# Optimization experiments

Measured on AMD Instinct MI355X. Metric: run time of the kernel, lower is better.

Reference implementation:

```python
import jax, jax.numpy as jnp
import numpy as np

TOP_K = 2  # module uses global top_k=2

def setup_inputs() -> dict:
    key = jax.random.key(0)
    k1, k2, k3 = jax.random.split(key, 3)
    B, S, D, E = 4, 4096, 2048, 64
    x = jax.random.normal(k1, (B, S, D), dtype=jnp.float32)
    W = jax.random.normal(k2, (E, D), dtype=jnp.float32) * 0.02  # gate_linear weight (no bias)
    noise_weight = jnp.zeros((E,), dtype=jnp.float32)  # nn.Parameter(torch.zeros(E))
    noise = jax.random.normal(k3, (B, S, E), dtype=jnp.float32)  # randn_like(logits) * noisy_std(=1.0)
    return {"x": x, "W": W, "noise_weight": noise_weight, "noise": noise}

def reference(x, W, noise_weight, noise):
    # logits = gate_linear(x)
    logits = jnp.einsum('bsd,ed->bse', x, W)
    # noisy logits: noise * noise_weight (per-expert scale), added to logits
    logits_noisy = logits + noise * noise_weight
    # top-k (largest, sorted descending, like torch.topk)
    top_vals, top_idx = jax.lax.top_k(logits_noisy, TOP_K)  # [B,S,k]
    B, S, E = logits_noisy.shape
    # scatter top-k values into -inf tensor along expert dim
    sparse = jnp.full_like(logits_noisy, -jnp.inf)
    b_ix = jnp.arange(B)[:, None, None]
    s_ix = jnp.arange(S)[None, :, None]
    sparse = sparse.at[b_ix, s_ix, top_idx].set(top_vals)
    # softmax over experts; exp(-inf)=0 zeros out non-selected experts
    gated_probs = jax.nn.softmax(sparse, axis=-1)
    return (gated_probs, top_idx, top_vals)
```

## Files before the change

### kernel.cpp

```cpp
#include <hip/hip_runtime.h>
#include <math.h>


typedef __attribute__((ext_vector_type(8))) __bf16 bf16x8;
typedef __attribute__((ext_vector_type(8))) unsigned short u16x8;
typedef __attribute__((ext_vector_type(4))) float f32x4;

constexpr int EXPN = 64;
constexpr int TM   = 16;
constexpr int BK   = 32;

__device__ __forceinline__ void split2(float f, unsigned short& h, unsigned short& l) {
    const unsigned b = __float_as_uint(f);
    h = (unsigned short)(b >> 16);
    const float fh = __uint_as_float(b & 0xffff0000u);
    l = (unsigned short)(__float_as_uint(f - fh) >> 16);
}

__device__ __forceinline__ bf16x8 as_bf16(u16x8 v) {
    union { u16x8 u; bf16x8 b; } c; c.u = v; return c.b;
}

__device__ __forceinline__ void gload16(const void* g, void* l) {
    typedef __attribute__((address_space(1))) void gv;
    typedef __attribute__((address_space(3))) void lv;
    __builtin_amdgcn_global_load_lds((gv*)g, (lv*)l, 16, 0, 0);
}

__global__ __launch_bounds__(256)
void convert_w_kernel(const float* __restrict__ W,
                      unsigned short* __restrict__ whp,
                      unsigned short* __restrict__ wlp, int n4)
{
    const int i = blockIdx.x * 256 + threadIdx.x;
    if (i >= n4) return;
    const float4 v = *(const float4*)(W + (size_t)i * 4);
    const float f[4] = {v.x, v.y, v.z, v.w};
    unsigned short h[4], l[4];
#pragma unroll
    for (int j = 0; j < 4; ++j) split2(f[j], h[j], l[j]);
    *(ushort4*)(whp + (size_t)i * 4) = make_ushort4(h[0], h[1], h[2], h[3]);
    *(ushort4*)(wlp + (size_t)i * 4) = make_ushort4(l[0], l[1], l[2], l[3]);
}

__global__ __launch_bounds__(256, 6)
void moe_gate_kernel(const float* __restrict__ x,
                     const float* __restrict__ W,
                     const unsigned short* __restrict__ whp,
                     const unsigned short* __restrict__ wlp,
                     const float* __restrict__ nw,
                     const float* __restrict__ noise,
                     float* __restrict__ probs,
                     float* __restrict__ idx_out,
                     float* __restrict__ val_out,
                     int D)
{
    __shared__ float          xs[2][TM][BK];
    __shared__ unsigned short ws[2][EXPN][2 * BK];
    __shared__ float          ls[TM][EXPN + 1];

    const int tid  = threadIdx.x;
    const int lane = tid & 63;
    const int wv   = tid >> 6;
    const int m0   = blockIdx.x * TM;

    const int fr = lane & 15;
    const int kq = (lane >> 4) * 8;
    const int er = wv * 16 + fr;

    const int sl8 = lane >> 3;
    const int gl  = lane & 7;
    const int j0 = wv * 2, j1 = j0 + 1;
    const int e0 = j0 * 8 + sl8, e1 = j1 * 8 + sl8;
    const int g0 = gl ^ (e0 & 7), g1 = gl ^ (e1 & 7);
    const unsigned short* wsrc0 = (g0 < 4)
        ? whp + (size_t)e0 * D + g0 * 8
        : wlp + (size_t)e0 * D + (g0 - 4) * 8;
    const unsigned short* wsrc1 = (g1 < 4)
        ? whp + (size_t)e1 * D + g1 * 8
        : wlp + (size_t)e1 * D + (g1 - 4) * 8;
    const float* xsrc = nullptr;
    if (wv >= 2) {
        const int row = (wv - 2) * 8 + sl8;
        const int gx  = gl ^ (row & 7);
        xsrc = x + (size_t)(m0 + row) * D + gx * 4;
    }

#define STAGE(b, c) {                                                        \
        gload16(wsrc0 + (size_t)(c) * BK, &ws[b][0][0] + j0 * 512);          \
        gload16(wsrc1 + (size_t)(c) * BK, &ws[b][0][0] + j1 * 512);          \
        if (wv >= 2)                                                         \
            gload16(xsrc + (size_t)(c) * BK, &xs[b][0][0] + (wv - 2) * 256); \
    }

    f32x4 acc = {0.f, 0.f, 0.f, 0.f};

#define COMPUTE(b) {                                                              \
        const char* xbp = (const char*)&xs[b][0][0];                              \
        const char* wbp = (const char*)&ws[b][0][0];                              \
        const float4 xa  = *(const float4*)(xbp + fr * 128 + (((kq >> 2)    ) ^ (fr & 7)) * 16); \
        const float4 xc  = *(const float4*)(xbp + fr * 128 + (((kq >> 2) + 1) ^ (fr & 7)) * 16); \
        const u16x8  bhv = *(const u16x8*)(wbp + er * 128 + (((kq >> 3)    ) ^ (fr & 7)) * 16); \
        const u16x8  blv = *(const u16x8*)(wbp + er * 128 + (((kq >> 3) + 4) ^ (fr & 7)) * 16); \
        const float xf[8] = {xa.x, xa.y, xa.z, xa.w, xc.x, xc.y, xc.z, xc.w};     \
        u16x8 hv, lv;                                                             \
        _Pragma("unroll")                                                         \
        for (int i_ = 0; i_ < 8; ++i_) {                                          \
            unsigned short h_, l_; split2(xf[i_], h_, l_);                        \
            hv[i_] = h_; lv[i_] = l_;                                             \
        }                                                                         \
        const bf16x8 ah = as_bf16(hv), al = as_bf16(lv);                          \
        acc = __builtin_amdgcn_mfma_f32_16x16x32_bf16(ah, as_bf16(bhv), acc, 0, 0, 0); \
        acc = __builtin_amdgcn_mfma_f32_16x16x32_bf16(ah, as_bf16(blv), acc, 0, 0, 0); \
        acc = __builtin_amdgcn_mfma_f32_16x16x32_bf16(al, as_bf16(bhv), acc, 0, 0, 0); \
    }

    const int nchunk = D / BK;
    STAGE(0, 0)
    __syncthreads();

    for (int c = 0; c < nchunk; ++c) {
        if (c & 1) {
            if (c + 1 < nchunk) STAGE(0, c + 1)
            COMPUTE(1)
        } else {
            if (c + 1 < nchunk) STAGE(1, c + 1)
            COMPUTE(0)
        }
        __syncthreads();
    }

#undef STAGE
#undef COMPUTE

    const int trow = (lane >> 4) * 4;
#pragma unroll
    for (int r = 0; r < 4; ++r)
        ls[trow + r][wv * 16 + fr] = acc[r];
    __syncthreads();

    const float nwv = nw[lane];

#pragma unroll 1
    for (int t = 0; t < 4; ++t) {
        const int tl = wv * 4 + t;
        const int g  = m0 + tl;
        const float logit = fmaf(noise[(size_t)g * EXPN + lane], nwv, ls[tl][lane]);

        float v0; int i0;
        {
            float v = logit; int ix = lane;
#pragma unroll
            for (int off = 32; off; off >>= 1) {
                const float vo = __shfl_xor(v, off);
                const int   io = __shfl_xor(ix, off);
                if (vo > v || (vo == v && io < ix)) { v = vo; ix = io; }
            }
            v0 = v; i0 = ix;
        }
        float v1; int i1;
        {
            float v = (lane == i0) ? -INFINITY : logit; int ix = lane;
#pragma unroll
            for (int off = 32; off; off >>= 1) {
                const float vo = __shfl_xor(v, off);
                const int   io = __shfl_xor(ix, off);
                if (vo > v || (vo == v && io < ix)) { v = vo; ix = io; }
            }
            v1 = v; i1 = ix;
        }
        float v2; int i2;
        {
            float v = (lane == i0 || lane == i1) ? -INFINITY : logit; int ix = lane;
#pragma unroll
            for (int off = 32; off; off >>= 1) {
                const float vo = __shfl_xor(v, off);
                const int   io = __shfl_xor(ix, off);
                if (vo > v || (vo == v && io < ix)) { v = vo; ix = io; }
            }
            v2 = v; i2 = ix;
        }

        const float eps = 1e-3f;
        if ((v0 - v1) < eps || (v1 - v2) < eps) {
            const float* xr  = x + (size_t)g * D;
            const float* w0r = W + (size_t)i0 * D;
            const float* w1r = W + (size_t)i1 * D;
            const float* w2r = W + (size_t)i2 * D;
            double s0 = 0.0, s1 = 0.0, s2 = 0.0;
            for (int d = lane; d < D; d += 64) {
                const double xv = (double)xr[d];
                s0 += xv * (double)w0r[d];
                s1 += xv * (double)w1r[d];
                s2 += xv * (double)w2r[d];
            }
#pragma unroll
            for (int off = 32; off; off >>= 1) {
                s0 += __shfl_xor(s0, off);
                s1 += __shfl_xor(s1, off);
                s2 += __shfl_xor(s2, off);
            }
            double d0 = s0 + (double)noise[(size_t)g * EXPN + i0] * (double)nw[i0];
            double d1 = s1 + (double)noise[(size_t)g * EXPN + i1] * (double)nw[i1];
            double d2 = s2 + (double)noise[(size_t)g * EXPN + i2] * (double)nw[i2];
            #define CSWAP(va, ia, vb, ib)                                   \
                if ((vb > va) || (vb == va && ib < ia)) {                   \
                    double tv = va; va = vb; vb = tv;                       \
                    int ti = ia; ia = ib; ib = ti; }
            CSWAP(d0, i0, d1, i1)
            CSWAP(d1, i1, d2, i2)
            CSWAP(d0, i0, d1, i1)
            #undef CSWAP
            v0 = (float)d0; v1 = (float)d1;
        }

        const float e1  = expf(v1 - v0);
        const float inv = 1.0f / (1.0f + e1);

        float p = 0.f;
        if (lane == i0)      p = inv;
        else if (lane == i1) p = e1 * inv;
        probs[(size_t)g * EXPN + lane] = p;

        if (lane == 0) {
            idx_out[(size_t)g * 2 + 0] = (float)i0;
            idx_out[(size_t)g * 2 + 1] = (float)i1;
            val_out[(size_t)g * 2 + 0] = v0;
            val_out[(size_t)g * 2 + 1] = v1;
        }
    }
}

extern "C" void kernel_launch(void* const* d_in, const int* in_sizes, int n_in,
                              void* d_out, int out_size, void* d_ws, size_t ws_size,
                              hipStream_t stream) {
    const float* x     = (const float*)d_in[0];
    const float* W     = (const float*)d_in[1];
    const float* nw    = (const float*)d_in[2];
    const float* noise = (const float*)d_in[3];

    const int M = in_sizes[3] / EXPN;
    const int D = in_sizes[0] / M;
    const int wn = in_sizes[1];

    unsigned short* whp = (unsigned short*)d_ws;
    unsigned short* wlp = whp + (size_t)wn;

    float* probs   = (float*)d_out;
    float* idx_out = probs + (size_t)M * EXPN;
    float* val_out = idx_out + (size_t)M * 2;

    const int n4 = wn / 4;
    convert_w_kernel<<<(n4 + 255) / 256, 256, 0, stream>>>(W, whp, wlp, n4);

    const int grid = M / TM;
    moe_gate_kernel<<<grid, 256, 0, stream>>>(x, W, whp, wlp, nw, noise,
                                              probs, idx_out, val_out, D);
}
```

Baseline: 256.8 us.

## Enlarge tiles, use 512-thread blocks, triple-buffer loads with vmcnt waits

Raises the row tile from 16 to 32 tokens and the K chunk from 32 to 64, and launches 512 threads per block (two token halves times four expert quarters). The double buffer with a full __syncthreads every chunk becomes a three-stage ring that keeps two chunks of global-to-LDS loads in flight, using explicit s_waitcnt vmcnt plus a bare barrier. The aim is to hide load latency better and halve the number of barriers. In exchange there are fewer blocks, more LDS per block and lower occupancy. The epilogue must also cover 32 rows, and part of that code is not visible.

After: 222.7 us. 13.3% less time.

```diff
diff --git a/kernel.cpp b/kernel.cpp
--- a/kernel.cpp
+++ b/kernel.cpp
@@ -7,8 +7,11 @@
 typedef __attribute__((ext_vector_type(4))) float f32x4;
 
 constexpr int EXPN = 64;
-constexpr int TM   = 16;
-constexpr int BK   = 32;
+constexpr int TM   = 32;
+constexpr int BK   = 64;
+constexpr int WBYTES = EXPN * 2 * BK * 2;
+constexpr int XBYTES = TM * BK * 4;
+constexpr int BUFB   = WBYTES + XBYTES;
 
 __device__ __forceinline__ void split2(float f, unsigned short& h, unsigned short& l) {
     const unsigned b = __float_as_uint(f);
@@ -43,7 +46,7 @@
     *(ushort4*)(wlp + (size_t)i * 4) = make_ushort4(l[0], l[1], l[2], l[3]);
 }
 
-__global__ __launch_bounds__(256, 6)
+__global__ __launch_bounds__(512, 4)
 void moe_gate_kernel(const float* __restrict__ x,
                      const float* __restrict__ W,
                      const unsigned short* __restrict__ whp,
@@ -55,88 +58,90 @@
                      float* __restrict__ val_out,
                      int D)
 {
-    __shared__ float          xs[2][TM][BK];
-    __shared__ unsigned short ws[2][EXPN][2 * BK];
-    __shared__ float          ls[TM][EXPN + 1];
+    __shared__ __align__(16) char smem[3 * BUFB];
 
     const int tid  = threadIdx.x;
     const int lane = tid & 63;
     const int wv   = tid >> 6;
+    const int th   = wv >> 2;
+    const int eq   = wv & 3;
     const int m0   = blockIdx.x * TM;
 
     const int fr = lane & 15;
     const int kq = (lane >> 4) * 8;
-    const int er = wv * 16 + fr;
-
-    const int sl8 = lane >> 3;
-    const int gl  = lane & 7;
+    const int f7 = fr & 7;
+
+    const int sl   = lane >> 4;
+    const int slot = lane & 15;
     const int j0 = wv * 2, j1 = j0 + 1;
-    const int e0 = j0 * 8 + sl8, e1 = j1 * 8 + sl8;
-    const int g0 = gl ^ (e0 & 7), g1 = gl ^ (e1 & 7);
-    const unsigned short* wsrc0 = (g0 < 4)
-        ? whp + (size_t)e0 * D + g0 * 8
-        : wlp + (size_t)e0 * D + (g0 - 4) * 8;
-    const unsigned short* wsrc1 = (g1 < 4)
-        ? whp + (size_t)e1 * D + g1 * 8
-        : wlp + (size_t)e1 * D + (g1 - 4) * 8;
-    const float* xsrc = nullptr;
-    if (wv >= 2) {
-        const int row = (wv - 2) * 8 + sl8;
-        const int gx  = gl ^ (row & 7);
-        xsrc = x + (size_t)(m0 + row) * D + gx * 4;
-    }
-
-#define STAGE(b, c) {                                                        \
-        gload16(wsrc0 + (size_t)(c) * BK, &ws[b][0][0] + j0 * 512);          \
-        gload16(wsrc1 + (size_t)(c) * BK, &ws[b][0][0] + j1 * 512);          \
-        if (wv >= 2)                                                         \
-            gload16(xsrc + (size_t)(c) * BK, &xs[b][0][0] + (wv - 2) * 256); \
+    const int we0 = j0 * 4 + sl, we1 = j1 * 4 + sl;
+    const int wg0 = slot ^ (we0 & 7), wg1 = slot ^ (we1 & 7);
+    const unsigned short* wsrc0 = ((wg0 < 8) ? whp : wlp)
+                                + (size_t)we0 * D + (wg0 & 7) * 8;
+    const unsigned short* wsrc1 = ((wg1 < 8) ? whp : wlp)
+                                + (size_t)we1 * D + (wg1 & 7) * 8;
+    const int xrow = wv * 4 + sl;
+    const int xg   = slot ^ (xrow & 7);
+    const float* xsrc = x + (size_t)(m0 + xrow) * D + xg * 4;
+
+#define STAGE(b, c) {                                                     \
+        char* bb_ = smem + (b) * BUFB;                                    \
+        gload16(wsrc0 + (size_t)(c) * BK, bb_ + j0 * 1024);               \
+        gload16(wsrc1 + (size_t)(c) * BK, bb_ + j1 * 1024);               \
+        gload16(xsrc  + (size_t)(c) * BK, bb_ + WBYTES + wv * 1024);      \
     }
 
     f32x4 acc = {0.f, 0.f, 0.f, 0.f};
 
 #define COMPUTE(b) {                                                              \
-        const char* xbp = (const char*)&xs[b][0][0];                              \
-        const char* wbp = (const char*)&ws[b][0][0];                              \
-        const float4 xa  = *(const float4*)(xbp + fr * 128 + (((kq >> 2)    ) ^ (fr & 7)) * 16); \
-        const float4 xc  = *(const float4*)(xbp + fr * 128 + (((kq >> 2) + 1) ^ (fr & 7)) * 16); \
-        const u16x8  bhv = *(const u16x8*)(wbp + er * 128 + (((kq >> 3)    ) ^ (fr & 7)) * 16); \
-        const u16x8  blv = *(const u16x8*)(wbp + er * 128 + (((kq >> 3) + 4) ^ (fr & 7)) * 16); \
-        const float xf[8] = {xa.x, xa.y, xa.z, xa.w, xc.x, xc.y, xc.z, xc.w};     \
-        u16x8 hv, lv;                                                             \
+        const char* wbp_ = smem + (b) * BUFB;                                     \
+        const char* xbp_ = wbp_ + WBYTES;                                         \
         _Pragma("unroll")                                                         \
-        for (int i_ = 0; i_ < 8; ++i_) {                                          \
-            unsigned short h_, l_; split2(xf[i_], h_, l_);                        \
-            hv[i_] = h_; lv[i_] = l_;                                             \
+        for (int ks_ = 0; ks_ < 2; ++ks_) {                                       \
+            const int kk_ = ks_ * 32 + kq;                                        \
+            const int sx_ = (kk_ >> 2) ^ f7;            \
+            const float4 xa_ = *(const float4*)(xbp_ + (th*16+fr)*256 + sx_*16);  \
+            const float4 xc_ = *(const float4*)(xbp_ + (th*16+fr)*256 + (sx_^1)*16); \
+            const int gh_ = kk_ >> 3;                                             \
+            const u16x8 bh_ = *(const u16x8*)(wbp_ + (eq*16+fr)*256 + (gh_ ^ f7)*16); \
+            const u16x8 bl_ = *(const u16x8*)(wbp_ + (eq*16+fr)*256 + (8 + (gh_ ^ f7))*16); \
+            const float xf_[8] = {xa_.x, xa_.y, xa_.z, xa_.w,                     \
+                                  xc_.x, xc_.y, xc_.z, xc_.w};                    \
+            u16x8 hv_, lv_;                                                       \
+            _Pragma("unroll")                                                     \
+            for (int i_ = 0; i_ < 8; ++i_) {                                      \
+                unsigned short h_, l_; split2(xf_[i_], h_, l_);                   \
+                hv_[i_] = h_; lv_[i_] = l_;                                       \
+            }                                                                     \
+            const bf16x8 ah_ = as_bf16(hv_), al_ = as_bf16(lv_);                  \
+            acc = __builtin_amdgcn_mfma_f32_16x16x32_bf16(ah_, as_bf16(bh_), acc, 0, 0, 0); \
+            acc = __builtin_amdgcn_mfma_f32_16x16x32_bf16(ah_, as_bf16(bl_), acc, 0, 0, 0); \
+            acc = __builtin_amdgcn_mfma_f32_16x16x32_bf16(al_, as_bf16(bh_), acc, 0, 0, 0); \
         }                                                                         \
-        const bf16x8 ah = as_bf16(hv), al = as_bf16(lv);                          \
-        acc = __builtin_amdgcn_mfma_f32_16x16x32_bf16(ah, as_bf16(bhv), acc, 0, 0, 0); \
-        acc = __builtin_amdgcn_mfma_f32_16x16x32_bf16(ah, as_bf16(blv), acc, 0, 0, 0); \
-        acc = __builtin_amdgcn_mfma_f32_16x16x32_bf16(al, as_bf16(bhv), acc, 0, 0, 0); \
     }
 
     const int nchunk = D / BK;
     STAGE(0, 0)
-    __syncthreads();
+    STAGE(1, 1)
 
     for (int c = 0; c < nchunk; ++c) {
-        if (c & 1) {
-            if (c + 1 < nchunk) STAGE(0, c + 1)
-            COMPUTE(1)
-        } else {
-            if (c + 1 < nchunk) STAGE(1, c + 1)
-            COMPUTE(0)
-        }
-        __syncthreads();
+        if (c < nchunk - 1) asm volatile("s_waitcnt vmcnt(3)" ::: "memory");
+        else                asm volatile("s_waitcnt vmcnt(0)" ::: "memory");
+        __builtin_amdgcn_s_barrier();
+        if (c + 2 < nchunk) STAGE((c + 2) % 3, c + 2)
+        COMPUTE(c % 3)
     }
 
 #undef STAGE
 #undef COMPUTE
 
-    const int trow = (lane >> 4) * 4;
+    __syncthreads();
+
+    float (*ls)[EXPN + 1] = (float (*)[EXPN + 1])smem;
+    const int trow = th * 16 + (lane >> 4) * 4;
 #pragma unroll
     for (int r = 0; r < 4; ++r)
-        ls[trow + r][wv * 16 + fr] = acc[r];
+        ls[trow + r][eq * 16 + fr] = acc[r];
     __syncthreads();
 
     const float nwv = nw[lane];
@@ -254,6 +259,6 @@
     convert_w_kernel<<<(n4 + 255) / 256, 256, 0, stream>>>(W, whp, wlp, n4);
 
     const int grid = M / TM;
-    moe_gate_kernel<<<grid, 256, 0, stream>>>(x, W, whp, wlp, nw, noise,
+    moe_gate_kernel<<<grid, 512, 0, stream>>>(x, W, whp, wlp, nw, noise,
                                               probs, idx_out, val_out, D);
 }
```

## Enlarge gate GEMM tile to 64 tokens with split-K across 16 waves

Applied to the files above, without the earlier changes.

Moves from 16-token, 4-wave blocks to 64-token, 1024-thread blocks. Each wave computes a 2x2 set of 16x16 MFMA tiles over one quarter of a 128-wide K chunk, and the four K-partials are reduced through shared memory at the end. The larger tile reuses each staged W chunk across four times as many tokens, cutting redundant W traffic and barrier count per FLOP. The bf16 hi/lo split of x now uses byte-permute packing. The costs are much more LDS per block, lower occupancy, and a full vmcnt drain at every barrier.

After: 215.1 us. -16.2%, faster.

```diff
diff --git a/kernel.cpp b/kernel.cpp
--- a/kernel.cpp
+++ b/kernel.cpp
@@ -5,10 +5,15 @@
 typedef __attribute__((ext_vector_type(8))) __bf16 bf16x8;
 typedef __attribute__((ext_vector_type(8))) unsigned short u16x8;
 typedef __attribute__((ext_vector_type(4))) float f32x4;
+typedef __attribute__((ext_vector_type(4))) unsigned u32x4;
 
 constexpr int EXPN = 64;
-constexpr int TM   = 16;
-constexpr int BK   = 32;
+constexpr int TM   = 64;
+constexpr int BK   = 128;
+constexpr int WCH  = EXPN * BK * 2 * 2;
+constexpr int XCH  = TM * BK * 4;
+constexpr int BUF  = WCH + XCH;
+constexpr int NBUF = 2;
 
 __device__ __forceinline__ void split2(float f, unsigned short& h, unsigned short& l) {
     const unsigned b = __float_as_uint(f);
@@ -19,6 +24,34 @@
 
 __device__ __forceinline__ bf16x8 as_bf16(u16x8 v) {
     union { u16x8 u; bf16x8 b; } c; c.u = v; return c.b;
+}
+__device__ __forceinline__ bf16x8 as_bf16_u32(u32x4 v) {
+    union { u32x4 u; bf16x8 b; } c; c.u = v; return c.b;
+}
+
+__device__ __forceinline__ void split_pack(float4 a, float4 c, bf16x8& hi, bf16x8& lo) {
+    const unsigned u0=__float_as_uint(a.x), u1=__float_as_uint(a.y),
+                   u2=__float_as_uint(a.z), u3=__float_as_uint(a.w),
+                   u4=__float_as_uint(c.x), u5=__float_as_uint(c.y),
+                   u6=__float_as_uint(c.z), u7=__float_as_uint(c.w);
+    u32x4 hp, lp;
+    hp[0] = __builtin_amdgcn_perm(u1, u0, 0x07060302u);
+    hp[1] = __builtin_amdgcn_perm(u3, u2, 0x07060302u);
+    hp[2] = __builtin_amdgcn_perm(u5, u4, 0x07060302u);
+    hp[3] = __builtin_amdgcn_perm(u7, u6, 0x07060302u);
+    const unsigned d0=__float_as_uint(a.x-__uint_as_float(u0&0xffff0000u));
+    const unsigned d1=__float_as_uint(a.y-__uint_as_float(u1&0xffff0000u));
+    const unsigned d2=__float_as_uint(a.z-__uint_as_float(u2&0xffff0000u));
+    const unsigned d3=__float_as_uint(a.w-__uint_as_float(u3&0xffff0000u));
+    const unsigned d4=__float_as_uint(c.x-__uint_as_float(u4&0xffff0000u));
+    const unsigned d5=__float_as_uint(c.y-__uint_as_float(u5&0xffff0000u));
+    const unsigned d6=__float_as_uint(c.z-__uint_as_float(u6&0xffff0000u));
+    const unsigned d7=__float_as_uint(c.w-__uint_as_float(u7&0xffff0000u));
+    lp[0] = __builtin_amdgcn_perm(d1, d0, 0x07060302u);
+    lp[1] = __builtin_amdgcn_perm(d3, d2, 0x07060302u);
+    lp[2] = __builtin_amdgcn_perm(d5, d4, 0x07060302u);
+    lp[3] = __builtin_amdgcn_perm(d7, d6, 0x07060302u);
+    hi = as_bf16_u32(hp); lo = as_bf16_u32(lp);
 }
 
 __device__ __forceinline__ void gload16(const void* g, void* l) {
@@ -43,7 +76,9 @@
     *(ushort4*)(wlp + (size_t)i * 4) = make_ushort4(l[0], l[1], l[2], l[3]);
 }
 
-__global__ __launch_bounds__(256, 6)
+#define MFMA16(a, b, c) __builtin_amdgcn_mfma_f32_16x16x32_bf16((a), (b), (c), 0, 0, 0)
+
+__global__ __launch_bounds__(1024, 4)
 void moe_gate_kernel(const float* __restrict__ x,
                      const float* __restrict__ W,
                      const unsigned short* __restrict__ whp,
@@ -55,88 +90,111 @@
                      float* __restrict__ val_out,
                      int D)
 {
-    __shared__ float          xs[2][TM][BK];
-    __shared__ unsigned short ws[2][EXPN][2 * BK];
-    __shared__ float          ls[TM][EXPN + 1];
+    __shared__ __align__(16) char smem[NBUF * BUF];
 
     const int tid  = threadIdx.x;
     const int lane = tid & 63;
     const int wv   = tid >> 6;
+    const int kw   = wv >> 2;
+    const int th   = (wv >> 1) & 1;
+    const int eh   = wv & 1;
     const int m0   = blockIdx.x * TM;
 
-    const int fr = lane & 15;
-    const int kq = (lane >> 4) * 8;
-    const int er = wv * 16 + fr;
-
-    const int sl8 = lane >> 3;
-    const int gl  = lane & 7;
-    const int j0 = wv * 2, j1 = j0 + 1;
-    const int e0 = j0 * 8 + sl8, e1 = j1 * 8 + sl8;
-    const int g0 = gl ^ (e0 & 7), g1 = gl ^ (e1 & 7);
-    const unsigned short* wsrc0 = (g0 < 4)
-        ? whp + (size_t)e0 * D + g0 * 8
-        : wlp + (size_t)e0 * D + (g0 - 4) * 8;
-    const unsigned short* wsrc1 = (g1 < 4)
-        ? whp + (size_t)e1 * D + g1 * 8
-        : wlp + (size_t)e1 * D + (g1 - 4) * 8;
-    const float* xsrc = nullptr;
-    if (wv >= 2) {
-        const int row = (wv - 2) * 8 + sl8;
-        const int gx  = gl ^ (row & 7);
-        xsrc = x + (size_t)(m0 + row) * D + gx * 4;
-    }
-
-#define STAGE(b, c) {                                                        \
-        gload16(wsrc0 + (size_t)(c) * BK, &ws[b][0][0] + j0 * 512);          \
-        gload16(wsrc1 + (size_t)(c) * BK, &ws[b][0][0] + j1 * 512);          \
-        if (wv >= 2)                                                         \
-            gload16(xsrc + (size_t)(c) * BK, &xs[b][0][0] + (wv - 2) * 256); \
-    }
-
-    f32x4 acc = {0.f, 0.f, 0.f, 0.f};
-
-#define COMPUTE(b) {                                                              \
-        const char* xbp = (const char*)&xs[b][0][0];                              \
-        const char* wbp = (const char*)&ws[b][0][0];                              \
-        const float4 xa  = *(const float4*)(xbp + fr * 128 + (((kq >> 2)    ) ^ (fr & 7)) * 16); \
-        const float4 xc  = *(const float4*)(xbp + fr * 128 + (((kq >> 2) + 1) ^ (fr & 7)) * 16); \
-        const u16x8  bhv = *(const u16x8*)(wbp + er * 128 + (((kq >> 3)    ) ^ (fr & 7)) * 16); \
-        const u16x8  blv = *(const u16x8*)(wbp + er * 128 + (((kq >> 3) + 4) ^ (fr & 7)) * 16); \
-        const float xf[8] = {xa.x, xa.y, xa.z, xa.w, xc.x, xc.y, xc.z, xc.w};     \
-        u16x8 hv, lv;                                                             \
-        _Pragma("unroll")                                                         \
-        for (int i_ = 0; i_ < 8; ++i_) {                                          \
-            unsigned short h_, l_; split2(xf[i_], h_, l_);                        \
-            hv[i_] = h_; lv[i_] = l_;                                             \
-        }                                                                         \
-        const bf16x8 ah = as_bf16(hv), al = as_bf16(lv);                          \
-        acc = __builtin_amdgcn_mfma_f32_16x16x32_bf16(ah, as_bf16(bhv), acc, 0, 0, 0); \
-        acc = __builtin_amdgcn_mfma_f32_16x16x32_bf16(ah, as_bf16(blv), acc, 0, 0, 0); \
-        acc = __builtin_amdgcn_mfma_f32_16x16x32_bf16(al, as_bf16(bhv), acc, 0, 0, 0); \
+    const int fr  = lane & 15;
+    const int khi = lane >> 4;
+
+    const int sub  = lane >> 5;
+    const int slot = lane & 31;
+    const int we0 = 4 * wv + sub, we1 = we0 + 2;
+    const int wg0 = (slot & ~7) | ((slot & 7) ^ (we0 & 7));
+    const int wg1 = (slot & ~7) | ((slot & 7) ^ (we1 & 7));
+    const unsigned short* wsrc0 = ((wg0 < 16) ? whp : wlp)
+                                + (size_t)we0 * D + (wg0 & 15) * 8;
+    const unsigned short* wsrc1 = ((wg1 < 16) ? whp : wlp)
+                                + (size_t)we1 * D + (wg1 & 15) * 8;
+    const int xt0 = 4 * wv + sub, xt1 = xt0 + 2;
+    const int xg0 = (slot & ~7) | ((slot & 7) ^ (xt0 & 7));
+    const int xg1 = (slot & ~7) | ((slot & 7) ^ (xt1 & 7));
+    const float* xsrc0 = x + (size_t)(m0 + xt0) * D + xg0 * 4;
+    const float* xsrc1 = x + (size_t)(m0 + xt1) * D + xg1 * 4;
+
+#define STAGE(b, c) {                                                     \
+        char* bb_ = smem + (b) * BUF;                                     \
+        gload16(wsrc0 + (size_t)(c) * BK, bb_ + wv * 2048);               \
+        gload16(wsrc1 + (size_t)(c) * BK, bb_ + wv * 2048 + 1024);        \
+        gload16(xsrc0 + (size_t)(c) * BK, bb_ + WCH + wv * 2048);         \
+        gload16(xsrc1 + (size_t)(c) * BK, bb_ + WCH + wv * 2048 + 1024);  \
+    }
+
+    f32x4 acc00 = {0.f,0.f,0.f,0.f};
+    f32x4 acc01 = {0.f,0.f,0.f,0.f};
+    f32x4 acc10 = {0.f,0.f,0.f,0.f};
+    f32x4 acc11 = {0.f,0.f,0.f,0.f};
+
+    const int t0 = th * 32 + fr, t1 = t0 + 16;
+    const int e0 = eh * 32 + fr, e1 = e0 + 16;
+    const int pa0 = kw * 8 + ((khi * 2)     ^ (t0 & 7));
+    const int pa1 = kw * 8 + ((khi * 2 + 1) ^ (t0 & 7));
+    const int gh  = kw * 4 + khi;
+    const int pb  = (gh & ~7) | ((gh & 7) ^ (e0 & 7));
+
+#define COMPUTE(b) {                                                            \
+        const char* wbp_ = smem + (b) * BUF;                                    \
+        const char* xbp_ = wbp_ + WCH;                                          \
+        const float4 xa0_ = *(const float4*)(xbp_ + t0 * 512 + pa0 * 16);       \
+        const float4 xc0_ = *(const float4*)(xbp_ + t0 * 512 + pa1 * 16);       \
+        const float4 xa1_ = *(const float4*)(xbp_ + t1 * 512 + pa0 * 16);       \
+        const float4 xc1_ = *(const float4*)(xbp_ + t1 * 512 + pa1 * 16);       \
+        const u16x8 bh0_ = *(const u16x8*)(wbp_ + e0 * 512 + pb * 16);          \
+        const u16x8 bl0_ = *(const u16x8*)(wbp_ + e0 * 512 + pb * 16 + 256);    \
+        const u16x8 bh1_ = *(const u16x8*)(wbp_ + e1 * 512 + pb * 16);          \
+        const u16x8 bl1_ = *(const u16x8*)(wbp_ + e1 * 512 + pb * 16 + 256);    \
+        bf16x8 ah0_, al0_, ah1_, al1_;                                          \
+        split_pack(xa0_, xc0_, ah0_, al0_);                                     \
+        split_pack(xa1_, xc1_, ah1_, al1_);                                     \
+        const bf16x8 h0_ = as_bf16(bh0_), l0_ = as_bf16(bl0_);                  \
+        const bf16x8 h1_ = as_bf16(bh1_), l1_ = as_bf16(bl1_);                  \
+        acc00 = MFMA16(ah0_, h0_, acc00);                                       \
+        acc00 = MFMA16(ah0_, l0_, acc00);                                       \
+        acc00 = MFMA16(al0_, h0_, acc00);                                       \
+        acc01 = MFMA16(ah0_, h1_, acc01);                                       \
+        acc01 = MFMA16(ah0_, l1_, acc01);                                       \
+        acc01 = MFMA16(al0_, h1_, acc01);                                       \
+        acc10 = MFMA16(ah1_, h0_, acc10);                                       \
+        acc10 = MFMA16(ah1_, l0_, acc10);                                       \
+        acc10 = MFMA16(al1_, h0_, acc10);                                       \
+        acc11 = MFMA16(ah1_, h1_, acc11);                                       \
+        acc11 = MFMA16(ah1_, l1_, acc11);                                       \
+        acc11 = MFMA16(al1_, h1_, acc11);                                       \
     }
 
     const int nchunk = D / BK;
     STAGE(0, 0)
-    __syncthreads();
 
     for (int c = 0; c < nchunk; ++c) {
-        if (c & 1) {
-            if (c + 1 < nchunk) STAGE(0, c + 1)
-            COMPUTE(1)
-        } else {
-            if (c + 1 < nchunk) STAGE(1, c + 1)
-            COMPUTE(0)
-        }
-        __syncthreads();
+        asm volatile("s_waitcnt lgkmcnt(0)" ::: "memory");
+        asm volatile("s_waitcnt vmcnt(0)" ::: "memory");
+        __builtin_amdgcn_s_barrier();
+        asm volatile("" ::: "memory");
+        if (c + 1 < nchunk) STAGE((c + 1) & 1, c + 1)
+        COMPUTE(c & 1)
     }
 
 #undef STAGE
 #undef COMPUTE
 
-    const int trow = (lane >> 4) * 4;
-#pragma unroll
-    for (int r = 0; r < 4; ++r)
-        ls[trow + r][wv * 16 + fr] = acc[r];
+    __syncthreads();
+
+    float (*pl)[TM][EXPN + 1] = (float (*)[TM][EXPN + 1])smem;
+    const int tr0 = th * 32 + khi * 4;
+    const int ec0 = eh * 32 + fr;
+#pragma unroll
+    for (int r = 0; r < 4; ++r) {
+        pl[kw][tr0 + r][ec0]           = acc00[r];
+        pl[kw][tr0 + r][ec0 + 16]      = acc01[r];
+        pl[kw][tr0 + 16 + r][ec0]      = acc10[r];
+        pl[kw][tr0 + 16 + r][ec0 + 16] = acc11[r];
+    }
     __syncthreads();
 
     const float nwv = nw[lane];
@@ -145,7 +203,9 @@
     for (int t = 0; t < 4; ++t) {
         const int tl = wv * 4 + t;
         const int g  = m0 + tl;
-        const float logit = fmaf(noise[(size_t)g * EXPN + lane], nwv, ls[tl][lane]);
+        const float lg = pl[0][tl][lane] + pl[1][tl][lane]
+                       + pl[2][tl][lane] + pl[3][tl][lane];
+        const float logit = fmaf(noise[(size_t)g * EXPN + lane], nwv, lg);
 
         float v0; int i0;
         {
@@ -254,6 +314,6 @@
     convert_w_kernel<<<(n4 + 255) / 256, 256, 0, stream>>>(W, whp, wlp, n4);
 
     const int grid = M / TM;
-    moe_gate_kernel<<<grid, 256, 0, stream>>>(x, W, whp, wlp, nw, noise,
-                                              probs, idx_out, val_out, D);
-}
+    moe_gate_kernel<<<grid, 1024, 0, stream>>>(x, W, whp, wlp, nw, noise,
+                                               probs, idx_out, val_out, D);
+}
```
